# Optimization experiments

Measured on AMD Instinct MI355X. Metric: run time of the kernel, lower is better.

## Reference

```python
import jax, jax.numpy as jnp
import numpy as np

C, D, K, N, R = 96, 192, 4, 16, 6  # d_model, d_inner, directions, d_state, dt_rank
B, H, W = 8, 64, 64


def _ln(x, w, b):
    mu = x.mean(-1, keepdims=True)
    var = ((x - mu) ** 2).mean(-1, keepdims=True)
    return (x - mu) * jax.lax.rsqrt(var + 1e-5) * w + b


def setup_inputs() -> dict:
    key = jax.random.key(0)
    ks = jax.random.split(key, 16)
    s = 0.02
    A = jnp.tile(jnp.arange(1, N + 1, dtype=jnp.float32)[None, None, :], (K, D, 1))
    return {
        "x": jax.random.normal(ks[0], (B, C, H, W), jnp.float32),
        "ln1_w": jnp.ones((C,), jnp.float32),
        "ln1_b": jnp.zeros((C,), jnp.float32),
        "in_proj_w": jax.random.normal(ks[1], (2 * D, C), jnp.float32) * s,
        "conv_w": jax.random.normal(ks[2], (D, 1, 3, 3), jnp.float32) * s,
        "conv_b": jnp.zeros((D,), jnp.float32),
        "x_proj_w": jax.random.normal(ks[3], (K, R + 2 * N, D), jnp.float32) * s,
        "dt_projs_w": jax.random.normal(ks[4], (K, D, R), jnp.float32) * s,
        "dt_projs_b": jax.random.normal(ks[5], (K, D), jnp.float32) * 0.1,
        "A_logs": jnp.log(A),
        "Ds": jnp.ones((K, D), jnp.float32),
        "out_norm_w": jnp.ones((D,), jnp.float32),
        "out_norm_b": jnp.zeros((D,), jnp.float32),
        "out_proj_w": jax.random.normal(ks[6], (C, D), jnp.float32) * s,
        "pm_norm_w": jnp.ones((4 * C,), jnp.float32),
        "pm_norm_b": jnp.zeros((4 * C,), jnp.float32),
        "pm_red_w": jax.random.normal(ks[7], (2 * C, 4 * C), jnp.float32) * s,
    }


def reference(x, ln1_w, ln1_b, in_proj_w, conv_w, conv_b, x_proj_w, dt_projs_w,
              dt_projs_b, A_logs, Ds, out_norm_w, out_norm_b, out_proj_w,
              pm_norm_w, pm_norm_b, pm_red_w):
    b, c, h, w = x.shape
    L = h * w
    xh = jnp.transpose(x, (0, 2, 3, 1))  # [B,H,W,C]
    resid = xh
    xn = _ln(xh, ln1_w, ln1_b)
    xz = xn @ in_proj_w.T  # [B,H,W,2D]
    xp, z = xz[..., :D], xz[..., D:]
    xc = jnp.transpose(xp, (0, 3, 1, 2))  # [B,D,H,W]
    xc = jax.lax.conv_general_dilated(
        xc, conv_w, (1, 1), ((1, 1), (1, 1)),
        dimension_numbers=("NCHW", "OIHW", "NCHW"), feature_group_count=D)
    xc = jax.nn.silu(xc + conv_b[None, :, None, None])
    # cross-scan: row-major, col-major, and their reverses -> [B,K,D,L]
    xf = xc.reshape(b, D, L)
    xt = jnp.transpose(xc, (0, 1, 3, 2)).reshape(b, D, L)
    xs = jnp.stack([xf, xt, xf[..., ::-1], xt[..., ::-1]], axis=1)
    x_dbl = jnp.einsum("bkdl,kcd->bkcl", xs, x_proj_w)
    dts = jnp.einsum("bkrl,kdr->bkdl", x_dbl[:, :, :R], dt_projs_w)
    Bs = x_dbl[:, :, R:R + N]  # [B,K,N,L]
    Cs = x_dbl[:, :, R + N:R + 2 * N]
    delta = jax.nn.softplus(dts + dt_projs_b[None, :, :, None])  # [B,K,D,L]
    A = -jnp.exp(A_logs)  # [K,D,N]
    dT = jnp.transpose(delta, (3, 0, 1, 2))  # [L,B,K,D]
    uT = jnp.transpose(xs, (3, 0, 1, 2))
    BT = jnp.transpose(Bs, (3, 0, 1, 2))  # [L,B,K,N]
    CT = jnp.transpose(Cs, (3, 0, 1, 2))
    h0 = jnp.zeros((b, K, D, N), x.dtype)

    def step(hst, inp):
        dt, ut, bt, ct = inp
        hst = hst * jnp.exp(dt[..., None] * A) + (dt * ut)[..., None] * bt[:, :, None, :]
        return hst, jnp.einsum("bkdn,bkn->bkd", hst, ct)

    _, yT = jax.lax.scan(step, h0, (dT, uT, BT, CT))  # yT: [L,B,K,D]
    y = jnp.transpose(yT, (1, 2, 3, 0)) + Ds[None, :, :, None] * xs  # [B,K,D,L]

    def unT(v):  # undo col-major traversal
        return jnp.transpose(v.reshape(b, D, w, h), (0, 1, 3, 2)).reshape(b, D, L)

    yc = y[:, 0] + y[:, 2, :, ::-1] + unT(y[:, 1]) + unT(y[:, 3, :, ::-1])
    yo = jnp.transpose(yc.reshape(b, D, h, w), (0, 2, 3, 1))  # [B,H,W,D]
    yo = _ln(yo, out_norm_w, out_norm_b) * jax.nn.silu(z)
    out = resid + yo @ out_proj_w.T  # [B,H,W,C]
    # PatchMerging2D
    x0 = out[:, 0::2, 0::2]
    x1 = out[:, 1::2, 0::2]
    x2 = out[:, 0::2, 1::2]
    x3 = out[:, 1::2, 1::2]
    xm = jnp.concatenate([x0, x1, x2, x3], -1)  # [B,H/2,W/2,4C]
    xm = _ln(xm, pm_norm_w, pm_norm_b) @ pm_red_w.T  # [B,H/2,W/2,2C]
    return jnp.transpose(xm, (0, 3, 1, 2))
```

## Files before the change

kernel.cpp:

```cpp
#include <hip/hip_runtime.h>
#include <hip/hip_bf16.h>


__device__ __forceinline__ float sigm(float x){ return 1.f/(1.f+__expf(-x)); }
__device__ __forceinline__ float softplus_(float x){ return (x>20.f)? x : __logf(1.f+__expf(x)); }

__device__ __forceinline__ int perm_kl(int k, int v){
  if(k==0) return v;
  if(k==1) return ((v&63)<<6)|(v>>6);
  if(k==2) return 4095-v;
  int m = 4095-v; return ((m&63)<<6)|(m>>6);
}

__global__ __launch_bounds__(256) void k0_prep(
    const float* __restrict__ ipw, const float* __restrict__ xpw,
    const float* __restrict__ dtw, const float* __restrict__ opw,
    const float* __restrict__ pmw,
    float* __restrict__ ipwT, float* __restrict__ xpwTp,
    float* __restrict__ dtwT, float* __restrict__ opwT,
    float* __restrict__ pmwT)
{
  int g = blockIdx.x*256 + threadIdx.x;
  if(g < 36864){
    int c = g/384, n = g%384;
    ipwT[g] = ipw[n*96 + c];
  } else if(g < 67584){
    int t = g - 36864; int dd = t/160, n = t - dd*160; int k = n/40, c = n - k*40;
    float v;
    if(c < 6)       v = xpw[(k*38 + c)*192 + dd];
    else if(c < 8)  v = 0.f;
    else            v = xpw[(k*38 + (c-2))*192 + dd];
    xpwTp[t] = v;
  } else if(g < 72192){
    int t = g - 67584; int kr = t/192, d = t - kr*192; int k = kr/6, r = kr - k*6;
    dtwT[t] = dtw[(k*192 + d)*6 + r];
  } else if(g < 90624){
    int t = g - 72192; int d = t/96, c = t - d*96;
    opwT[t] = opw[c*192 + d];
  } else if(g < 164352){
    int t = g - 90624; int n = t/192, c2 = t - n*192;
    pmwT[t] = pmw[c2*384 + n];
  }
}

#define XT_PAD 68
__global__ __launch_bounds__(256) void k1_ln_inproj(
    const float* __restrict__ x, const float* __restrict__ lnw, const float* __restrict__ lnb,
    const float* __restrict__ ipwT, float* __restrict__ xT,
    float* __restrict__ xp, float* __restrict__ z)
{
  __shared__ float xt[96*XT_PAD];
  __shared__ float lnw_s[96], lnb_s[96], mu_s[64], rs_s[64];
  int tid = threadIdx.x;
  int mt = blockIdx.x, nt = blockIdx.y, b = blockIdx.z;
  int g0 = mt*64;
  const float* xb = x + (size_t)b*96*4096 + g0;
  for(int idx=tid; idx<6144; idx+=256){
    int c = idx>>6, p = idx&63;
    xt[c*XT_PAD+p] = xb[c*4096 + p];
  }
  if(tid<96){ lnw_s[tid]=lnw[tid]; lnb_s[tid]=lnb[tid]; }
  __syncthreads();
  if(nt==0){
    float* xTb = xT + ((size_t)(b*4096 + g0))*96;
    for(int idx=tid; idx<6144; idx+=256){
      int p = idx/96, c = idx - p*96;
      xTb[idx] = xt[c*XT_PAD+p];
    }
  }
  if(tid<64){
    float s=0.f,q=0.f;
    for(int c=0;c<96;c++){ float v=xt[c*XT_PAD+tid]; s+=v; q+=v*v; }
    float mu = s*(1.f/96.f);
    mu_s[tid]=mu; rs_s[tid]=rsqrtf(q*(1.f/96.f)-mu*mu+1e-5f);
  }
  __syncthreads();
  for(int idx=tid; idx<6144; idx+=256){
    int c = idx>>6, p = idx&63;
    int a = c*XT_PAD+p;
    xt[a] = (xt[a]-mu_s[p])*rs_s[p]*lnw_s[c]+lnb_s[c];
  }
  __syncthreads();
  int tm = tid>>5, tn = tid&31;
  float acc[8][4];
  #pragma unroll
  for(int i=0;i<8;i++){acc[i][0]=0.f;acc[i][1]=0.f;acc[i][2]=0.f;acc[i][3]=0.f;}
  const float* wbase = ipwT + nt*128 + tn*4;
  for(int kk=0;kk<96;kk++){
    float4 w4 = *(const float4*)(wbase + kk*384);
    float4 a0 = *(const float4*)&xt[kk*XT_PAD + tm*8];
    float4 a1 = *(const float4*)&xt[kk*XT_PAD + tm*8 + 4];
    float av[8]={a0.x,a0.y,a0.z,a0.w,a1.x,a1.y,a1.z,a1.w};
    #pragma unroll
    for(int i=0;i<8;i++){
      acc[i][0]=fmaf(av[i],w4.x,acc[i][0]);
      acc[i][1]=fmaf(av[i],w4.y,acc[i][1]);
      acc[i][2]=fmaf(av[i],w4.z,acc[i][2]);
      acc[i][3]=fmaf(av[i],w4.w,acc[i][3]);
    }
  }
  int n = nt*128 + tn*4;
  #pragma unroll
  for(int i=0;i<8;i++){
    size_t row = (size_t)(b*4096 + g0 + tm*8 + i);
    float4 v = make_float4(acc[i][0],acc[i][1],acc[i][2],acc[i][3]);
    if(n < 192) *(float4*)(xp + row*192 + n) = v;
    else        *(float4*)(z  + row*192 + (n-192)) = v;
  }
}

__global__ __launch_bounds__(192) void k2_conv(
    const float* __restrict__ xp, const float* __restrict__ cw, const float* __restrict__ cb,
    float* __restrict__ xc)
{
  __shared__ float cw_s[1728];
  int tid = threadIdx.x;
  int pq = blockIdx.x, b = blockIdx.y;
  for(int i=tid;i<1728;i+=192) cw_s[i]=cw[i];
  __syncthreads();
  int p0 = pq*4;
  int h = p0>>6, w0 = p0&63;
  const float* base = xp + (size_t)b*4096*192 + tid;
  const float* wp = &cw_s[tid*9];
  float bias = cb[tid];
  float acc[4] = {bias,bias,bias,bias};
  #pragma unroll
  for(int ky=0;ky<3;ky++){
    int hh = h+ky-1;
    if(hh<0||hh>63) continue;
    float v[6];
    #pragma unroll
    for(int xx=0;xx<6;xx++){
      int ww = w0-1+xx;
      v[xx] = (ww>=0 && ww<64) ? base[((size_t)(hh*64+ww))*192] : 0.f;
    }
    float wk0=wp[ky*3], wk1=wp[ky*3+1], wk2=wp[ky*3+2];
    #pragma unroll
    for(int j=0;j<4;j++)
      acc[j] = fmaf(v[j],wk0, fmaf(v[j+1],wk1, fmaf(v[j+2],wk2, acc[j])));
  }
  #pragma unroll
  for(int j=0;j<4;j++){
    float a = acc[j];
    a = a * sigm(a);
    xc[((size_t)(b*4096)+p0+j)*192 + tid] = a;
  }
}

__global__ __launch_bounds__(320) void k3_proj(
    const float* __restrict__ xc, const float* __restrict__ xpwTp,
    float* __restrict__ xdbl)
{
  __shared__ float sm[32*192];
  int tid = threadIdx.x;
  int mt = blockIdx.x, b = blockIdx.y;
  int g0 = mt*32;
  const float* xcb = xc + ((size_t)(b*4096 + g0))*192;
  for(int idx=tid; idx<6144; idx+=320) sm[idx] = xcb[idx];
  __syncthreads();
  int tn = tid%40, tm = tid/40;
  float acc[4][4];
  #pragma unroll
  for(int i=0;i<4;i++){acc[i][0]=0.f;acc[i][1]=0.f;acc[i][2]=0.f;acc[i][3]=0.f;}
  const float* wb = xpwTp + tn*4;
  for(int kk=0;kk<192;kk+=2){
    float4 w0 = *(const float4*)(wb + kk*160);
    float4 w1 = *(const float4*)(wb + (kk+1)*160);
    #pragma unroll
    for(int i=0;i<4;i++){
      float2 a = *(const float2*)&sm[(tm*4+i)*192 + kk];
      acc[i][0] = fmaf(a.x,w0.x, fmaf(a.y,w1.x, acc[i][0]));
      acc[i][1] = fmaf(a.x,w0.y, fmaf(a.y,w1.y, acc[i][1]));
      acc[i][2] = fmaf(a.x,w0.z, fmaf(a.y,w1.z, acc[i][2]));
      acc[i][3] = fmaf(a.x,w0.w, fmaf(a.y,w1.w, acc[i][3]));
    }
  }
  #pragma unroll
  for(int i=0;i<4;i++){
    *(float4*)(xdbl + ((size_t)(b*4096 + g0 + tm*4 + i))*160 + tn*4)
      = make_float4(acc[i][0],acc[i][1],acc[i][2],acc[i][3]);
  }
}

__global__ __launch_bounds__(192) void k4a_scanlocal(
    const float* __restrict__ xdbl, const float* __restrict__ xc,
    const float* __restrict__ alog, const float* __restrict__ dtwT,
    const float* __restrict__ dtb,
    float* __restrict__ localH, float* __restrict__ decayT)
{
  int d = threadIdx.x;
  int ch = blockIdx.x, k = blockIdx.y, b = blockIdx.z;
  __shared__ float dtw_s[6*192];
  #pragma unroll
  for(int r=0;r<6;r++) dtw_s[r*192+d] = dtwT[(k*6+r)*192+d];
  __syncthreads();
  float A[16];
  {
    const float4* ap = (const float4*)(alog + (k*192+d)*16);
    float4 a0=ap[0],a1=ap[1],a2=ap[2],a3=ap[3];
    float t[16]={a0.x,a0.y,a0.z,a0.w,a1.x,a1.y,a1.z,a1.w,a2.x,a2.y,a2.z,a2.w,a3.x,a3.y,a3.z,a3.w};
    #pragma unroll
    for(int n=0;n<16;n++) A[n] = -__expf(t[n]);
  }
  bool fast = true;
  #pragma unroll
  for(int n=1;n<16;n++)
    fast = fast && (fabsf(A[n] - (float)(n+1)*A[0]) <= 1e-4f*(float)(n+1)*fabsf(A[0]));
  float dtbv = dtb[k*192+d];
  float h[16];
  #pragma unroll
  for(int n=0;n<16;n++) h[n]=0.f;
  float S=0.f;
  const float* xb = xc + (size_t)b*4096*192 + d;
  size_t prow = (size_t)b*4096;
  for(int i=0;i<64;i++){
    int p = perm_kl(k, ch*64+i);
    const float* row = xdbl + (prow+p)*160 + k*40;
    float u = xb[(size_t)p*192];
    float delta = dtbv;
    #pragma unroll
    for(int r=0;r<6;r++) delta = fmaf(row[r], dtw_s[r*192+d], delta);
    delta = softplus_(delta);
    float4 B0=*(const float4*)(row+8),  B1=*(const float4*)(row+12),
           B2=*(const float4*)(row+16), B3=*(const float4*)(row+20);
    float Bn[16]={B0.x,B0.y,B0.z,B0.w,B1.x,B1.y,B1.z,B1.w,B2.x,B2.y,B2.z,B2.w,B3.x,B3.y,B3.z,B3.w};
    float du = delta*u;
    S += delta;
    if(fast){
      float e1 = __expf(delta*A[0]);
      float e = e1;
      #pragma unroll
      for(int n=0;n<16;n++){ h[n] = fmaf(h[n], e, du*Bn[n]); e *= e1; }
    } else {
      #pragma unroll
      for(int n=0;n<16;n++) h[n] = fmaf(h[n], __expf(delta*A[n]), du*Bn[n]);
    }
  }
  float dec[16];
  if(fast){
    float s1 = __expf(S*A[0]);
    float e = s1;
    #pragma unroll
    for(int n=0;n<16;n++){ dec[n]=e; e*=s1; }
  } else {
    #pragma unroll
    for(int n=0;n<16;n++) dec[n] = __expf(A[n]*S);
  }
  float* lh = localH + ((((size_t)(b*4+k))*64 + ch)*192 + d)*16;
  float* dt = decayT + ((((size_t)(b*4+k))*64 + ch)*192 + d)*16;
  #pragma unroll
  for(int n4=0;n4<4;n4++){
    *(float4*)(lh + n4*4) = make_float4(h[n4*4],h[n4*4+1],h[n4*4+2],h[n4*4+3]);
    *(float4*)(dt + n4*4) = make_float4(dec[n4*4],dec[n4*4+1],dec[n4*4+2],dec[n4*4+3]);
  }
}

__global__ __launch_bounds__(256) void k4b_chain(
    float* __restrict__ localH, const float* __restrict__ decayT)
{
  int g = blockIdx.x*256 + threadIdx.x;
  int bk = g/3072, dn = g - bk*3072;
  float hv = 0.f;
  size_t base = (size_t)bk*64*3072 + dn;
  for(int ch=0; ch<64; ch++){
    size_t idx = base + (size_t)ch*3072;
    float loc = localH[idx], dec = decayT[idx];
    localH[idx] = hv;
    hv = fmaf(hv, dec, loc);
  }
}

__global__ __launch_bounds__(192) void k4c_scanfull(
    const float* __restrict__ xdbl, const float* __restrict__ xc,
    const float* __restrict__ alog, const float* __restrict__ dtwT,
    const float* __restrict__ dtb, const float* __restrict__ hin,
    const float* __restrict__ Dsv, float* __restrict__ yB)
{
  int d = threadIdx.x;
  int ch = blockIdx.x, k = blockIdx.y, b = blockIdx.z;
  __shared__ float dtw_s[6*192];
  #pragma unroll
  for(int r=0;r<6;r++) dtw_s[r*192+d] = dtwT[(k*6+r)*192+d];
  __syncthreads();
  float A[16];
  {
    const float4* ap = (const float4*)(alog + (k*192+d)*16);
    float4 a0=ap[0],a1=ap[1],a2=ap[2],a3=ap[3];
    float t[16]={a0.x,a0.y,a0.z,a0.w,a1.x,a1.y,a1.z,a1.w,a2.x,a2.y,a2.z,a2.w,a3.x,a3.y,a3.z,a3.w};
    #pragma unroll
    for(int n=0;n<16;n++) A[n] = -__expf(t[n]);
  }
  bool fast = true;
  #pragma unroll
  for(int n=1;n<16;n++)
    fast = fast && (fabsf(A[n] - (float)(n+1)*A[0]) <= 1e-4f*(float)(n+1)*fabsf(A[0]));
  float dtbv = dtb[k*192+d];
  float h[16];
  {
    const float4* hp = (const float4*)(hin + ((((size_t)(b*4+k))*64 + ch)*192 + d)*16);
    float4 h0=hp[0],h1=hp[1],h2=hp[2],h3=hp[3];
    h[0]=h0.x;h[1]=h0.y;h[2]=h0.z;h[3]=h0.w;h[4]=h1.x;h[5]=h1.y;h[6]=h1.z;h[7]=h1.w;
    h[8]=h2.x;h[9]=h2.y;h[10]=h2.z;h[11]=h2.w;h[12]=h3.x;h[13]=h3.y;h[14]=h3.z;h[15]=h3.w;
  }
  float dsv = Dsv[k*192+d];
  const float* xb = xc + (size_t)b*4096*192 + d;
  size_t prow = (size_t)b*4096;
  size_t rbase = ((size_t)(b*4+k))*4096 + ch*64;
  float* yP = yB + rbase*192 + d;
  for(int i=0;i<64;i++){
    int p = perm_kl(k, ch*64+i);
    const float* row = xdbl + (prow+p)*160 + k*40;
    float u = xb[(size_t)p*192];
    float delta = dtbv;
    #pragma unroll
    for(int r=0;r<6;r++) delta = fmaf(row[r], dtw_s[r*192+d], delta);
    delta = softplus_(delta);
    float4 B0=*(const float4*)(row+8),  B1=*(const float4*)(row+12),
           B2=*(const float4*)(row+16), B3=*(const float4*)(row+20);
    float Bn[16]={B0.x,B0.y,B0.z,B0.w,B1.x,B1.y,B1.z,B1.w,B2.x,B2.y,B2.z,B2.w,B3.x,B3.y,B3.z,B3.w};
    float4 C0=*(const float4*)(row+24), C1=*(const float4*)(row+28),
           C2=*(const float4*)(row+32), C3=*(const float4*)(row+36);
    float Cn[16]={C0.x,C0.y,C0.z,C0.w,C1.x,C1.y,C1.z,C1.w,C2.x,C2.y,C2.z,C2.w,C3.x,C3.y,C3.z,C3.w};
    float du = delta*u;
    float y = 0.f;
    if(fast){
      float e1 = __expf(delta*A[0]);
      float e = e1;
      #pragma unroll
      for(int n=0;n<16;n++){ h[n] = fmaf(h[n], e, du*Bn[n]); y = fmaf(h[n], Cn[n], y); e *= e1; }
    } else {
      #pragma unroll
      for(int n=0;n<16;n++){ h[n] = fmaf(h[n], __expf(delta*A[n]), du*Bn[n]); y = fmaf(h[n], Cn[n], y); }
    }
    yP[(size_t)i*192] = fmaf(dsv, u, y);
  }
}

#define YPAD 193
__global__ __launch_bounds__(256) void k5_combine(
    const float* __restrict__ yS, const float* __restrict__ z, const float* __restrict__ xT,
    const float* __restrict__ onw, const float* __restrict__ onb,
    const float* __restrict__ opwT, float* __restrict__ out_pre)
{
  __shared__ float yn[64*YPAD];
  __shared__ float wsm[48*96];
  __shared__ float mu_s[64], rs_s[64];
  int tid = threadIdx.x;
  int mt = blockIdx.x, b = blockIdx.y;
  int g0 = mt*64;
  size_t base = (size_t)b*4*4096;
  for(int idx=tid; idx<12288; idx+=256){
    int p = idx/192, d = idx - p*192;
    int gp = g0 + p;
    int l1 = ((gp&63)<<6)|(gp>>6);
    float v = yS[(base + gp)*192 + d]
            + yS[(base + 4096 + l1)*192 + d]
            + yS[(base + 2*4096 + (4095-gp))*192 + d]
            + yS[(base + 3*4096 + (4095-l1))*192 + d];
    yn[p*YPAD+d] = v;
  }
  __syncthreads();
  {
    int p = tid>>2, q = tid&3;
    float s=0.f, sq=0.f;
    for(int c=q;c<192;c+=4){ float v=yn[p*YPAD+c]; s+=v; sq=fmaf(v,v,sq); }
    s  += __shfl_xor(s,1);  sq += __shfl_xor(sq,1);
    s  += __shfl_xor(s,2);  sq += __shfl_xor(sq,2);
    if(q==0){
      float mu = s*(1.f/192.f);
      mu_s[p]=mu; rs_s[p]=rsqrtf(sq*(1.f/192.f)-mu*mu+1e-5f);
    }
  }
  __syncthreads();
  for(int idx=tid; idx<12288; idx+=256){
    int p = idx/192, d = idx - p*192;
    float zz = z[((size_t)(b*4096+g0+p))*192 + d];
    float v = (yn[p*YPAD+d]-mu_s[p])*rs_s[p]*onw[d]+onb[d];
    yn[p*YPAD+d] = v * zz * sigm(zz);
  }
  __syncthreads();
  int tn = tid&15, tm = tid>>4;
  float acc[4][6];
  #pragma unroll
  for(int i=0;i<4;i++)
    #pragma unroll
    for(int j=0;j<6;j++) acc[i][j]=0.f;
  for(int kc=0; kc<4; kc++){
    for(int idx=tid; idx<4608; idx+=256) wsm[idx] = opwT[kc*4608 + idx];
    __syncthreads();
    for(int kk=0;kk<48;kk++){
      float a0 = yn[(tm*4+0)*YPAD + kc*48+kk];
      float a1 = yn[(tm*4+1)*YPAD + kc*48+kk];
      float a2 = yn[(tm*4+2)*YPAD + kc*48+kk];
      float a3 = yn[(tm*4+3)*YPAD + kc*48+kk];
      const float* wr = &wsm[kk*96 + tn*6];
      #pragma unroll
      for(int j=0;j<6;j++){
        float w = wr[j];
        acc[0][j]=fmaf(a0,w,acc[0][j]);
        acc[1][j]=fmaf(a1,w,acc[1][j]);
        acc[2][j]=fmaf(a2,w,acc[2][j]);
        acc[3][j]=fmaf(a3,w,acc[3][j]);
      }
    }
    __syncthreads();
  }
  #pragma unroll
  for(int i=0;i<4;i++){
    size_t row = (size_t)(b*4096 + g0 + tm*4 + i);
    const float* xr = xT + row*96 + tn*6;
    float* orr = out_pre + row*96 + tn*6;
    #pragma unroll
    for(int j=0;j<6;j++) orr[j] = acc[i][j] + xr[j];
  }
}

__global__ __launch_bounds__(192) void k6_pm(
    const float* __restrict__ out_pre, const float* __restrict__ pmw, const float* __restrict__ pmb,
    const float* __restrict__ pmwT, float* __restrict__ outp)
{
  __shared__ float xm[8*388];
  __shared__ float xo[8*193];
  __shared__ float mus[8], rss[8];
  int tid = threadIdx.x;
  int jt = blockIdx.x, i = blockIdx.y, b = blockIdx.z;
  for(int idx=tid; idx<3072; idx+=192){
    int pj = idx/384, n = idx - pj*384;
    int q = n/96, c = n - q*96;
    int j = jt*8 + pj;
    int h2 = 2*i + (q&1), w2 = 2*j + (q>>1);
    xm[pj*388+n] = out_pre[((size_t)b*4096 + h2*64 + w2)*96 + c];
  }
  __syncthreads();
  if(tid<8){
    float s=0.f,q=0.f;
    for(int n=0;n<384;n++){ float v=xm[tid*388+n]; s+=v; q+=v*v; }
    float mu=s*(1.f/384.f);
    mus[tid]=mu; rss[tid]=rsqrtf(q*(1.f/384.f)-mu*mu+1e-5f);
  }
  __syncthreads();
  for(int idx=tid; idx<3072; idx+=192){
    int pj = idx/384, n = idx - pj*384;
    xm[pj*388+n] = (xm[pj*388+n]-mus[pj])*rss[pj]*pmw[n]+pmb[n];
  }
  __syncthreads();
  float acc[8];
  #pragma unroll
  for(int pj=0;pj<8;pj++) acc[pj]=0.f;
  const float* wb = pmwT + tid;
  for(int n4=0;n4<96;n4++){
    float w0=wb[(n4*4+0)*192], w1=wb[(n4*4+1)*192], w2=wb[(n4*4+2)*192], w3=wb[(n4*4+3)*192];
    #pragma unroll
    for(int pj=0;pj<8;pj++){
      float4 v = *(const float4*)&xm[pj*388 + n4*4];
      acc[pj] = fmaf(v.x,w0,fmaf(v.y,w1,fmaf(v.z,w2,fmaf(v.w,w3,acc[pj]))));
    }
  }
  #pragma unroll
  for(int pj=0;pj<8;pj++) xo[pj*193+tid]=acc[pj];
  __syncthreads();
  for(int idx=tid; idx<1536; idx+=192){
    int c2 = idx>>3, pj = idx&7;
    outp[(((size_t)b*192 + c2)*32 + i)*32 + jt*8 + pj] = xo[pj*193+c2];
  }
}

extern "C" void kernel_launch(void* const* d_in, const int* in_sizes, int n_in,
                              void* d_out, int out_size, void* d_ws, size_t ws_size,
                              hipStream_t stream)
{
  const float* x    = (const float*)d_in[0];
  const float* lnw  = (const float*)d_in[1];
  const float* lnb  = (const float*)d_in[2];
  const float* ipw  = (const float*)d_in[3];
  const float* cw   = (const float*)d_in[4];
  const float* cb   = (const float*)d_in[5];
  const float* xpw  = (const float*)d_in[6];
  const float* dtw  = (const float*)d_in[7];
  const float* dtb  = (const float*)d_in[8];
  const float* alog = (const float*)d_in[9];
  const float* Dsv  = (const float*)d_in[10];
  const float* onw  = (const float*)d_in[11];
  const float* onb  = (const float*)d_in[12];
  const float* opw  = (const float*)d_in[13];
  const float* pmnw = (const float*)d_in[14];
  const float* pmnb = (const float*)d_in[15];
  const float* pmrw = (const float*)d_in[16];
  float* out = (float*)d_out;

  float* ws    = (float*)d_ws;
  float* xT    = ws;
  float* xpb   = xT + 3145728;
  float* zb    = xpb + 6291456;
  float* xcb   = zb + 6291456;
  float* yB    = xcb + 6291456;
  float* lH    = yB + 25165824;
  float* dT    = lH + 6291456;
  float* ipwT  = dT + 6291456;
  float* xpwTp = ipwT + 36864;
  float* dtwT  = xpwTp + 30720;
  float* opwT  = dtwT + 4608;
  float* pmwT  = opwT + 18432;
  float* xdbl  = xpb;
  float* outp  = xpb;

  k0_prep      <<<dim3(642),     dim3(256), 0, stream>>>(ipw,xpw,dtw,opw,pmrw, ipwT,xpwTp,dtwT,opwT,pmwT);
  k1_ln_inproj <<<dim3(64,3,8),  dim3(256), 0, stream>>>(x,lnw,lnb,ipwT, xT,xpb,zb);
  k2_conv      <<<dim3(1024,8),  dim3(192), 0, stream>>>(xpb,cw,cb, xcb);
  k3_proj      <<<dim3(128,8),   dim3(320), 0, stream>>>(xcb,xpwTp, xdbl);
  k4a_scanlocal<<<dim3(64,4,8),  dim3(192), 0, stream>>>(xdbl,xcb,alog,dtwT,dtb, lH,dT);
  k4b_chain    <<<dim3(384),     dim3(256), 0, stream>>>(lH,dT);
  k4c_scanfull <<<dim3(64,4,8),  dim3(192), 0, stream>>>(xdbl,xcb,alog,dtwT,dtb,lH,Dsv, yB);
  k5_combine   <<<dim3(64,8),    dim3(256), 0, stream>>>(yB,zb,xT,onw,onb,opwT, outp);
  k6_pm        <<<dim3(4,32,8),  dim3(192), 0, stream>>>(outp,pmnw,pmnb,pmwT, out);
}
```

Measured before the change: 359.8 us.

## Stage scan rows in shared memory, prefetch u, and shorten exp/dot dependency chains

Both chunked scan kernels now cooperatively load their 64 permuted x_dbl rows (dt, B, C) into shared memory up front, rather than each thread re-reading them from global memory. u values are prefetched four steps ahead, and the dt weights are held in registers. The serial power chain for the decay factors is replaced by a log-depth expansion, and the C dot product is split into four partial sums. This targets per-step global-load latency and long serial FMA dependency chains. In exchange it uses more registers and shared memory, which could reduce occupancy.

```diff
diff --git a/kernel.cpp b/kernel.cpp
--- a/kernel.cpp
+++ b/kernel.cpp
@@ -182,18 +182,30 @@
   }
 }
 
+#define EXPAND_E(e, f1)                                                     \
+    float f2=(f1)*(f1), f4=f2*f2, f8=f4*f4;                                 \
+    e[0]=(f1); e[1]=f2; e[2]=f2*(f1); e[3]=f4; e[4]=f4*(f1); e[5]=f4*f2;    \
+    e[6]=f4*e[2]; e[7]=f8; e[8]=f8*(f1); e[9]=f8*f2; e[10]=f8*e[2];         \
+    e[11]=f8*f4; e[12]=f8*e[4]; e[13]=f8*e[5]; e[14]=f8*e[6]; e[15]=f8*f8;
+
 __global__ __launch_bounds__(192) void k4a_scanlocal(
     const float* __restrict__ xdbl, const float* __restrict__ xc,
     const float* __restrict__ alog, const float* __restrict__ dtwT,
     const float* __restrict__ dtb,
     float* __restrict__ localH, float* __restrict__ decayT)
 {
+  __shared__ float rows[64*40];
   int d = threadIdx.x;
   int ch = blockIdx.x, k = blockIdx.y, b = blockIdx.z;
-  __shared__ float dtw_s[6*192];
-  #pragma unroll
-  for(int r=0;r<6;r++) dtw_s[r*192+d] = dtwT[(k*6+r)*192+d];
-  __syncthreads();
+  size_t prow = (size_t)b*4096;
+  for(int idx=d; idx<2560; idx+=192){
+    int i = idx/40, c = idx - i*40;
+    int p = perm_kl(k, ch*64+i);
+    rows[idx] = xdbl[(prow+p)*160 + k*40 + c];
+  }
+  float w0=dtwT[(k*6+0)*192+d], w1=dtwT[(k*6+1)*192+d], w2=dtwT[(k*6+2)*192+d],
+        w3=dtwT[(k*6+3)*192+d], w4=dtwT[(k*6+4)*192+d], w5=dtwT[(k*6+5)*192+d];
+  float dtbv = dtb[k*192+d];
   float A[16];
   {
     const float4* ap = (const float4*)(alog + (k*192+d)*16);
@@ -206,42 +218,52 @@
   #pragma unroll
   for(int n=1;n<16;n++)
     fast = fast && (fabsf(A[n] - (float)(n+1)*A[0]) <= 1e-4f*(float)(n+1)*fabsf(A[0]));
-  float dtbv = dtb[k*192+d];
   float h[16];
   #pragma unroll
   for(int n=0;n<16;n++) h[n]=0.f;
   float S=0.f;
   const float* xb = xc + (size_t)b*4096*192 + d;
-  size_t prow = (size_t)b*4096;
-  for(int i=0;i<64;i++){
-    int p = perm_kl(k, ch*64+i);
-    const float* row = xdbl + (prow+p)*160 + k*40;
-    float u = xb[(size_t)p*192];
-    float delta = dtbv;
-    #pragma unroll
-    for(int r=0;r<6;r++) delta = fmaf(row[r], dtw_s[r*192+d], delta);
-    delta = softplus_(delta);
-    float4 B0=*(const float4*)(row+8),  B1=*(const float4*)(row+12),
-           B2=*(const float4*)(row+16), B3=*(const float4*)(row+20);
-    float Bn[16]={B0.x,B0.y,B0.z,B0.w,B1.x,B1.y,B1.z,B1.w,B2.x,B2.y,B2.z,B2.w,B3.x,B3.y,B3.z,B3.w};
-    float du = delta*u;
-    S += delta;
-    if(fast){
-      float e1 = __expf(delta*A[0]);
-      float e = e1;
+  float u[4];
+  #pragma unroll
+  for(int j=0;j<4;j++) u[j] = xb[(size_t)perm_kl(k,ch*64+j)*192];
+  __syncthreads();
+  for(int ib=0; ib<64; ib+=4){
+    float nu[4]={0.f,0.f,0.f,0.f};
+    if(ib<60){
       #pragma unroll
-      for(int n=0;n<16;n++){ h[n] = fmaf(h[n], e, du*Bn[n]); e *= e1; }
-    } else {
+      for(int j=0;j<4;j++) nu[j] = xb[(size_t)perm_kl(k,ch*64+ib+4+j)*192];
+    }
+    #pragma unroll
+    for(int j=0;j<4;j++){
+      const float* row = &rows[(ib+j)*40];
+      float p01 = fmaf(row[1],w1, row[0]*w0);
+      float p23 = fmaf(row[3],w3, row[2]*w2);
+      float p45 = fmaf(row[5],w5, row[4]*w4);
+      float delta = softplus_((dtbv + p01) + (p23 + p45));
+      float du = delta*u[j];
+      S += delta;
+      float4 B0=*(const float4*)(row+8),  B1=*(const float4*)(row+12),
+             B2=*(const float4*)(row+16), B3=*(const float4*)(row+20);
+      float Bn[16]={B0.x,B0.y,B0.z,B0.w,B1.x,B1.y,B1.z,B1.w,
+                    B2.x,B2.y,B2.z,B2.w,B3.x,B3.y,B3.z,B3.w};
+      float e[16];
+      if(fast){
+        float f1=__expf(delta*A[0]);
+        EXPAND_E(e, f1)
+      } else {
+        #pragma unroll
+        for(int n=0;n<16;n++) e[n]=__expf(delta*A[n]);
+      }
       #pragma unroll
-      for(int n=0;n<16;n++) h[n] = fmaf(h[n], __expf(delta*A[n]), du*Bn[n]);
-    }
+      for(int n=0;n<16;n++) h[n] = fmaf(h[n], e[n], du*Bn[n]);
+    }
+    #pragma unroll
+    for(int j=0;j<4;j++) u[j]=nu[j];
   }
   float dec[16];
   if(fast){
     float s1 = __expf(S*A[0]);
-    float e = s1;
-    #pragma unroll
-    for(int n=0;n<16;n++){ dec[n]=e; e*=s1; }
+    EXPAND_E(dec, s1)
   } else {
     #pragma unroll
     for(int n=0;n<16;n++) dec[n] = __expf(A[n]*S);
@@ -276,12 +298,18 @@
     const float* __restrict__ dtb, const float* __restrict__ hin,
     const float* __restrict__ Dsv, float* __restrict__ yB)
 {
+  __shared__ float rows[64*40];
   int d = threadIdx.x;
   int ch = blockIdx.x, k = blockIdx.y, b = blockIdx.z;
-  __shared__ float dtw_s[6*192];
-  #pragma unroll
-  for(int r=0;r<6;r++) dtw_s[r*192+d] = dtwT[(k*6+r)*192+d];
-  __syncthreads();
+  size_t prow = (size_t)b*4096;
+  for(int idx=d; idx<2560; idx+=192){
+    int i = idx/40, c = idx - i*40;
+    int p = perm_kl(k, ch*64+i);
+    rows[idx] = xdbl[(prow+p)*160 + k*40 + c];
+  }
+  float w0=dtwT[(k*6+0)*192+d], w1=dtwT[(k*6+1)*192+d], w2=dtwT[(k*6+2)*192+d],
+        w3=dtwT[(k*6+3)*192+d], w4=dtwT[(k*6+4)*192+d], w5=dtwT[(k*6+5)*192+d];
+  float dtbv = dtb[k*192+d];
   float A[16];
   {
     const float4* ap = (const float4*)(alog + (k*192+d)*16);
@@ -294,7 +322,6 @@
   #pragma unroll
   for(int n=1;n<16;n++)
     fast = fast && (fabsf(A[n] - (float)(n+1)*A[0]) <= 1e-4f*(float)(n+1)*fabsf(A[0]));
-  float dtbv = dtb[k*192+d];
   float h[16];
   {
     const float4* hp = (const float4*)(hin + ((((size_t)(b*4+k))*64 + ch)*192 + d)*16);
@@ -304,35 +331,58 @@
   }
   float dsv = Dsv[k*192+d];
   const float* xb = xc + (size_t)b*4096*192 + d;
-  size_t prow = (size_t)b*4096;
   size_t rbase = ((size_t)(b*4+k))*4096 + ch*64;
   float* yP = yB + rbase*192 + d;
-  for(int i=0;i<64;i++){
-    int p = perm_kl(k, ch*64+i);
-    const float* row = xdbl + (prow+p)*160 + k*40;
-    float u = xb[(size_t)p*192];
-    float delta = dtbv;
-    #pragma unroll
-    for(int r=0;r<6;r++) delta = fmaf(row[r], dtw_s[r*192+d], delta);
-    delta = softplus_(delta);
-    float4 B0=*(const float4*)(row+8),  B1=*(const float4*)(row+12),
-           B2=*(const float4*)(row+16), B3=*(const float4*)(row+20);
-    float Bn[16]={B0.x,B0.y,B0.z,B0.w,B1.x,B1.y,B1.z,B1.w,B2.x,B2.y,B2.z,B2.w,B3.x,B3.y,B3.z,B3.w};
-    float4 C0=*(const float4*)(row+24), C1=*(const float4*)(row+28),
-           C2=*(const float4*)(row+32), C3=*(const float4*)(row+36);
-    float Cn[16]={C0.x,C0.y,C0.z,C0.w,C1.x,C1.y,C1.z,C1.w,C2.x,C2.y,C2.z,C2.w,C3.x,C3.y,C3.z,C3.w};
-    float du = delta*u;
-    float y = 0.f;
-    if(fast){
-      float e1 = __expf(delta*A[0]);
-      float e = e1;
+  float u[4];
+  #pragma unroll
+  for(int j=0;j<4;j++) u[j] = xb[(size_t)perm_kl(k,ch*64+j)*192];
+  __syncthreads();
+  float S=0.f;
+  for(int ib=0; ib<64; ib+=4){
+    float nu[4]={0.f,0.f,0.f,0.f};
+    if(ib<60){
       #pragma unroll
-      for(int n=0;n<16;n++){ h[n] = fmaf(h[n], e, du*Bn[n]); y = fmaf(h[n], Cn[n], y); e *= e1; }
-    } else {
+      for(int j=0;j<4;j++) nu[j] = xb[(size_t)perm_kl(k,ch*64+ib+4+j)*192];
+    }
+    #pragma unroll
+    for(int j=0;j<4;j++){
+      const float* row = &rows[(ib+j)*40];
+      float p01 = fmaf(row[1],w1, row[0]*w0);
+      float p23 = fmaf(row[3],w3, row[2]*w2);
+      float p45 = fmaf(row[5],w5, row[4]*w4);
+      float delta = softplus_((dtbv + p01) + (p23 + p45));
+      float du = delta*u[j];
+      S += delta;
+      float4 B0=*(const float4*)(row+8),  B1=*(const float4*)(row+12),
+             B2=*(const float4*)(row+16), B3=*(const float4*)(row+20);
+      float Bn[16]={B0.x,B0.y,B0.z,B0.w,B1.x,B1.y,B1.z,B1.w,
+                    B2.x,B2.y,B2.z,B2.w,B3.x,B3.y,B3.z,B3.w};
+      float4 C0=*(const float4*)(row+24), C1=*(const float4*)(row+28),
+             C2=*(const float4*)(row+32), C3=*(const float4*)(row+36);
+      float Cn[16]={C0.x,C0.y,C0.z,C0.w,C1.x,C1.y,C1.z,C1.w,
+                    C2.x,C2.y,C2.z,C2.w,C3.x,C3.y,C3.z,C3.w};
+      float e[16];
+      if(fast){
+        float f1=__expf(delta*A[0]);
+        EXPAND_E(e, f1)
+      } else {
+        #pragma unroll
+        for(int n=0;n<16;n++) e[n]=__expf(delta*A[n]);
+      }
       #pragma unroll
-      for(int n=0;n<16;n++){ h[n] = fmaf(h[n], __expf(delta*A[n]), du*Bn[n]); y = fmaf(h[n], Cn[n], y); }
-    }
-    yP[(size_t)i*192] = fmaf(dsv, u, y);
+      for(int n=0;n<16;n++) h[n] = fmaf(h[n], e[n], du*Bn[n]);
+      float y0=0.f,y1=0.f,y2=0.f,y3=0.f;
+      #pragma unroll
+      for(int n=0;n<4;n++){
+        y0 = fmaf(h[n],    Cn[n],    y0);
+        y1 = fmaf(h[n+4],  Cn[n+4],  y1);
+        y2 = fmaf(h[n+8],  Cn[n+8],  y2);
+        y3 = fmaf(h[n+12], Cn[n+12], y3);
+      }
+      yP[(size_t)(ib+j)*192] = fmaf(dsv, u[j], (y0+y1)+(y2+y3));
+    }
+    #pragma unroll
+    for(int j=0;j<4;j++) u[j]=nu[j];
   }
 }
 
```

New measurement: 430.4 us. +19.6%, slower.

## Stage per-chunk xdbl rows in shared memory and shorten scan dependency chains

Applied to the files above, without the earlier changes.

Both scan kernels now copy the chunk's 64 xdbl rows (40 floats each) into shared memory cooperatively before the loop, instead of every thread reading the same rows from global memory. The permutation is replaced by a start offset plus stride, so the u pointer advances by a fixed step. The dt weights move into registers. In the fast path the power chain for the decay is split into four parallel chains and the y reduction into four partial sums, which shortens the serial dependency latency. The cost is more shared memory per block and duplicated fast and slow loop bodies.

```diff
diff --git a/kernel.cpp b/kernel.cpp
--- a/kernel.cpp
+++ b/kernel.cpp
@@ -5,11 +5,13 @@
 __device__ __forceinline__ float sigm(float x){ return 1.f/(1.f+__expf(-x)); }
 __device__ __forceinline__ float softplus_(float x){ return (x>20.f)? x : __logf(1.f+__expf(x)); }
 
-__device__ __forceinline__ int perm_kl(int k, int v){
-  if(k==0) return v;
-  if(k==1) return ((v&63)<<6)|(v>>6);
-  if(k==2) return 4095-v;
-  int m = 4095-v; return ((m&63)<<6)|(m>>6);
+__device__ __forceinline__ void scan_p0dp(int k, int ch, int& p0, int& dp){
+  switch(k){
+    case 0:  p0 = ch*64;        dp = 1;   break;
+    case 1:  p0 = ch;           dp = 64;  break;
+    case 2:  p0 = 4095 - ch*64; dp = -1;  break;
+    default: p0 = 4095 - ch;    dp = -64; break;
+  }
 }
 
 __global__ __launch_bounds__(256) void k0_prep(
@@ -188,61 +190,100 @@
     const float* __restrict__ dtb,
     float* __restrict__ localH, float* __restrict__ decayT)
 {
+  __shared__ float rows[64*40];
   int d = threadIdx.x;
   int ch = blockIdx.x, k = blockIdx.y, b = blockIdx.z;
-  __shared__ float dtw_s[6*192];
-  #pragma unroll
-  for(int r=0;r<6;r++) dtw_s[r*192+d] = dtwT[(k*6+r)*192+d];
-  __syncthreads();
-  float A[16];
+  size_t prow = (size_t)b*4096;
+  int p0, dp;
+  scan_p0dp(k, ch, p0, dp);
+  for(int idx4=d; idx4<640; idx4+=192){
+    int i = idx4/10, c4 = idx4 - i*10;
+    *(float4*)&rows[idx4*4] =
+      *(const float4*)(xdbl + (prow + (size_t)(p0 + i*dp))*160 + k*40 + c4*4);
+  }
+  float w0=dtwT[(k*6+0)*192+d], w1=dtwT[(k*6+1)*192+d], w2=dtwT[(k*6+2)*192+d],
+        w3=dtwT[(k*6+3)*192+d], w4=dtwT[(k*6+4)*192+d], w5=dtwT[(k*6+5)*192+d];
+  float dtbv = dtb[k*192+d];
+  float A0; bool fast = true;
   {
-    const float4* ap = (const float4*)(alog + (k*192+d)*16);
+    const float4* ap = (const float4*)(alog + (size_t)(k*192+d)*16);
     float4 a0=ap[0],a1=ap[1],a2=ap[2],a3=ap[3];
     float t[16]={a0.x,a0.y,a0.z,a0.w,a1.x,a1.y,a1.z,a1.w,a2.x,a2.y,a2.z,a2.w,a3.x,a3.y,a3.z,a3.w};
-    #pragma unroll
-    for(int n=0;n<16;n++) A[n] = -__expf(t[n]);
-  }
-  bool fast = true;
-  #pragma unroll
-  for(int n=1;n<16;n++)
-    fast = fast && (fabsf(A[n] - (float)(n+1)*A[0]) <= 1e-4f*(float)(n+1)*fabsf(A[0]));
-  float dtbv = dtb[k*192+d];
+    A0 = -__expf(t[0]);
+    #pragma unroll
+    for(int n=1;n<16;n++)
+      fast = fast && (fabsf(-__expf(t[n]) - (float)(n+1)*A0) <= 1e-4f*(float)(n+1)*fabsf(A0));
+  }
   float h[16];
   #pragma unroll
   for(int n=0;n<16;n++) h[n]=0.f;
   float S=0.f;
-  const float* xb = xc + (size_t)b*4096*192 + d;
-  size_t prow = (size_t)b*4096;
-  for(int i=0;i<64;i++){
-    int p = perm_kl(k, ch*64+i);
-    const float* row = xdbl + (prow+p)*160 + k*40;
-    float u = xb[(size_t)p*192];
-    float delta = dtbv;
-    #pragma unroll
-    for(int r=0;r<6;r++) delta = fmaf(row[r], dtw_s[r*192+d], delta);
-    delta = softplus_(delta);
-    float4 B0=*(const float4*)(row+8),  B1=*(const float4*)(row+12),
-           B2=*(const float4*)(row+16), B3=*(const float4*)(row+20);
-    float Bn[16]={B0.x,B0.y,B0.z,B0.w,B1.x,B1.y,B1.z,B1.w,B2.x,B2.y,B2.z,B2.w,B3.x,B3.y,B3.z,B3.w};
-    float du = delta*u;
-    S += delta;
-    if(fast){
-      float e1 = __expf(delta*A[0]);
-      float e = e1;
+  const float* xu = xc + (prow + (size_t)p0)*192 + d;
+  ptrdiff_t ustride = (ptrdiff_t)dp*192;
+  float dec[16];
+  __syncthreads();
+  if(fast){
+    for(int i=0;i<64;i++){
+      const float* row = &rows[i*40];
+      float u = *xu; xu += ustride;
+      float p01 = fmaf(row[1],w1, row[0]*w0);
+      float p23 = fmaf(row[3],w3, row[2]*w2);
+      float p45 = fmaf(row[5],w5, row[4]*w4);
+      float delta = softplus_((dtbv + p01) + (p23 + p45));
+      float du = delta*u;
+      S += delta;
+      float4 B0=*(const float4*)(row+8),  B1=*(const float4*)(row+12),
+             B2=*(const float4*)(row+16), B3=*(const float4*)(row+20);
+      float e1=__expf(delta*A0);
+      float e2=e1*e1;
+      float c0=e1, c1=e2, c2=e2*e1, e4=e2*e2, c3=e4;
+      h[0]=fmaf(h[0],c0,du*B0.x); h[1]=fmaf(h[1],c1,du*B0.y);
+      h[2]=fmaf(h[2],c2,du*B0.z); h[3]=fmaf(h[3],c3,du*B0.w);
+      c0*=e4; c1*=e4; c2*=e4; c3*=e4;
+      h[4]=fmaf(h[4],c0,du*B1.x); h[5]=fmaf(h[5],c1,du*B1.y);
+      h[6]=fmaf(h[6],c2,du*B1.z); h[7]=fmaf(h[7],c3,du*B1.w);
+      c0*=e4; c1*=e4; c2*=e4; c3*=e4;
+      h[8]=fmaf(h[8],c0,du*B2.x); h[9]=fmaf(h[9],c1,du*B2.y);
+      h[10]=fmaf(h[10],c2,du*B2.z); h[11]=fmaf(h[11],c3,du*B2.w);
+      c0*=e4; c1*=e4; c2*=e4; c3*=e4;
+      h[12]=fmaf(h[12],c0,du*B3.x); h[13]=fmaf(h[13],c1,du*B3.y);
+      h[14]=fmaf(h[14],c2,du*B3.z); h[15]=fmaf(h[15],c3,du*B3.w);
+    }
+    float s1=__expf(S*A0);
+    float s2=s1*s1;
+    float c0=s1, c1=s2, c2=s2*s1, s4=s2*s2, c3=s4;
+    dec[0]=c0; dec[1]=c1; dec[2]=c2; dec[3]=c3;
+    c0*=s4; c1*=s4; c2*=s4; c3*=s4;
+    dec[4]=c0; dec[5]=c1; dec[6]=c2; dec[7]=c3;
+    c0*=s4; c1*=s4; c2*=s4; c3*=s4;
+    dec[8]=c0; dec[9]=c1; dec[10]=c2; dec[11]=c3;
+    c0*=s4; c1*=s4; c2*=s4; c3*=s4;
+    dec[12]=c0; dec[13]=c1; dec[14]=c2; dec[15]=c3;
+  } else {
+    float A[16];
+    {
+      const float4* ap = (const float4*)(alog + (size_t)(k*192+d)*16);
+      float4 a0=ap[0],a1=ap[1],a2=ap[2],a3=ap[3];
+      float t[16]={a0.x,a0.y,a0.z,a0.w,a1.x,a1.y,a1.z,a1.w,a2.x,a2.y,a2.z,a2.w,a3.x,a3.y,a3.z,a3.w};
       #pragma unroll
-      for(int n=0;n<16;n++){ h[n] = fmaf(h[n], e, du*Bn[n]); e *= e1; }
-    } else {
+      for(int n=0;n<16;n++) A[n] = -__expf(t[n]);
+    }
+    for(int i=0;i<64;i++){
+      const float* row = &rows[i*40];
+      float u = *xu; xu += ustride;
+      float p01 = fmaf(row[1],w1, row[0]*w0);
+      float p23 = fmaf(row[3],w3, row[2]*w2);
+      float p45 = fmaf(row[5],w5, row[4]*w4);
+      float delta = softplus_((dtbv + p01) + (p23 + p45));
+      float du = delta*u;
+      S += delta;
+      float4 B0=*(const float4*)(row+8),  B1=*(const float4*)(row+12),
+             B2=*(const float4*)(row+16), B3=*(const float4*)(row+20);
+      float Bn[16]={B0.x,B0.y,B0.z,B0.w,B1.x,B1.y,B1.z,B1.w,
+                    B2.x,B2.y,B2.z,B2.w,B3.x,B3.y,B3.z,B3.w};
       #pragma unroll
       for(int n=0;n<16;n++) h[n] = fmaf(h[n], __expf(delta*A[n]), du*Bn[n]);
     }
-  }
-  float dec[16];
-  if(fast){
-    float s1 = __expf(S*A[0]);
-    float e = s1;
-    #pragma unroll
-    for(int n=0;n<16;n++){ dec[n]=e; e*=s1; }
-  } else {
     #pragma unroll
     for(int n=0;n<16;n++) dec[n] = __expf(A[n]*S);
   }
@@ -276,25 +317,30 @@
     const float* __restrict__ dtb, const float* __restrict__ hin,
     const float* __restrict__ Dsv, float* __restrict__ yB)
 {
+  __shared__ float rows[64*40];
   int d = threadIdx.x;
   int ch = blockIdx.x, k = blockIdx.y, b = blockIdx.z;
-  __shared__ float dtw_s[6*192];
-  #pragma unroll
-  for(int r=0;r<6;r++) dtw_s[r*192+d] = dtwT[(k*6+r)*192+d];
-  __syncthreads();
-  float A[16];
+  size_t prow = (size_t)b*4096;
+  int p0, dp;
+  scan_p0dp(k, ch, p0, dp);
+  for(int idx4=d; idx4<640; idx4+=192){
+    int i = idx4/10, c4 = idx4 - i*10;
+    *(float4*)&rows[idx4*4] =
+      *(const float4*)(xdbl + (prow + (size_t)(p0 + i*dp))*160 + k*40 + c4*4);
+  }
+  float w0=dtwT[(k*6+0)*192+d], w1=dtwT[(k*6+1)*192+d], w2=dtwT[(k*6+2)*192+d],
+        w3=dtwT[(k*6+3)*192+d], w4=dtwT[(k*6+4)*192+d], w5=dtwT[(k*6+5)*192+d];
+  float dtbv = dtb[k*192+d];
+  float A0; bool fast = true;
   {
-    const float4* ap = (const float4*)(alog + (k*192+d)*16);
+    const float4* ap = (const float4*)(alog + (size_t)(k*192+d)*16);
     float4 a0=ap[0],a1=ap[1],a2=ap[2],a3=ap[3];
     float t[16]={a0.x,a0.y,a0.z,a0.w,a1.x,a1.y,a1.z,a1.w,a2.x,a2.y,a2.z,a2.w,a3.x,a3.y,a3.z,a3.w};
-    #pragma unroll
-    for(int n=0;n<16;n++) A[n] = -__expf(t[n]);
-  }
-  bool fast = true;
-  #pragma unroll
-  for(int n=1;n<16;n++)
-    fast = fast && (fabsf(A[n] - (float)(n+1)*A[0]) <= 1e-4f*(float)(n+1)*fabsf(A[0]));
-  float dtbv = dtb[k*192+d];
+    A0 = -__expf(t[0]);
+    #pragma unroll
+    for(int n=1;n<16;n++)
+      fast = fast && (fabsf(-__expf(t[n]) - (float)(n+1)*A0) <= 1e-4f*(float)(n+1)*fabsf(A0));
+  }
   float h[16];
   {
     const float4* hp = (const float4*)(hin + ((((size_t)(b*4+k))*64 + ch)*192 + d)*16);
@@ -303,36 +349,76 @@
     h[8]=h2.x;h[9]=h2.y;h[10]=h2.z;h[11]=h2.w;h[12]=h3.x;h[13]=h3.y;h[14]=h3.z;h[15]=h3.w;
   }
   float dsv = Dsv[k*192+d];
-  const float* xb = xc + (size_t)b*4096*192 + d;
-  size_t prow = (size_t)b*4096;
-  size_t rbase = ((size_t)(b*4+k))*4096 + ch*64;
-  float* yP = yB + rbase*192 + d;
-  for(int i=0;i<64;i++){
-    int p = perm_kl(k, ch*64+i);
-    const float* row = xdbl + (prow+p)*160 + k*40;
-    float u = xb[(size_t)p*192];
-    float delta = dtbv;
-    #pragma unroll
-    for(int r=0;r<6;r++) delta = fmaf(row[r], dtw_s[r*192+d], delta);
-    delta = softplus_(delta);
-    float4 B0=*(const float4*)(row+8),  B1=*(const float4*)(row+12),
-           B2=*(const float4*)(row+16), B3=*(const float4*)(row+20);
-    float Bn[16]={B0.x,B0.y,B0.z,B0.w,B1.x,B1.y,B1.z,B1.w,B2.x,B2.y,B2.z,B2.w,B3.x,B3.y,B3.z,B3.w};
-    float4 C0=*(const float4*)(row+24), C1=*(const float4*)(row+28),
-           C2=*(const float4*)(row+32), C3=*(const float4*)(row+36);
-    float Cn[16]={C0.x,C0.y,C0.z,C0.w,C1.x,C1.y,C1.z,C1.w,C2.x,C2.y,C2.z,C2.w,C3.x,C3.y,C3.z,C3.w};
-    float du = delta*u;
-    float y = 0.f;
-    if(fast){
-      float e1 = __expf(delta*A[0]);
-      float e = e1;
+  const float* xu = xc + (prow + (size_t)p0)*192 + d;
+  ptrdiff_t ustride = (ptrdiff_t)dp*192;
+  float* yP = yB + (((size_t)(b*4+k))*4096 + ch*64)*192 + d;
+  __syncthreads();
+  if(fast){
+    for(int i=0;i<64;i++){
+      const float* row = &rows[i*40];
+      float u = *xu; xu += ustride;
+      float p01 = fmaf(row[1],w1, row[0]*w0);
+      float p23 = fmaf(row[3],w3, row[2]*w2);
+      float p45 = fmaf(row[5],w5, row[4]*w4);
+      float delta = softplus_((dtbv + p01) + (p23 + p45));
+      float du = delta*u;
+      float4 B0=*(const float4*)(row+8),  B1=*(const float4*)(row+12),
+             B2=*(const float4*)(row+16), B3=*(const float4*)(row+20);
+      float4 C0=*(const float4*)(row+24), C1=*(const float4*)(row+28),
+             C2=*(const float4*)(row+32), C3=*(const float4*)(row+36);
+      float e1=__expf(delta*A0);
+      float e2=e1*e1;
+      float c0=e1, c1=e2, c2=e2*e1, e4=e2*e2, c3=e4;
+      h[0]=fmaf(h[0],c0,du*B0.x); h[1]=fmaf(h[1],c1,du*B0.y);
+      h[2]=fmaf(h[2],c2,du*B0.z); h[3]=fmaf(h[3],c3,du*B0.w);
+      float y0 = fmaf(h[0],C0.x, fmaf(h[1],C0.y, fmaf(h[2],C0.z, h[3]*C0.w)));
+      c0*=e4; c1*=e4; c2*=e4; c3*=e4;
+      h[4]=fmaf(h[4],c0,du*B1.x); h[5]=fmaf(h[5],c1,du*B1.y);
+      h[6]=fmaf(h[6],c2,du*B1.z); h[7]=fmaf(h[7],c3,du*B1.w);
+      float y1 = fmaf(h[4],C1.x, fmaf(h[5],C1.y, fmaf(h[6],C1.z, h[7]*C1.w)));
+      c0*=e4; c1*=e4; c2*=e4; c3*=e4;
+      h[8]=fmaf(h[8],c0,du*B2.x); h[9]=fmaf(h[9],c1,du*B2.y);
+      h[10]=fmaf(h[10],c2,du*B2.z); h[11]=fmaf(h[11],c3,du*B2.w);
+      float y2 = fmaf(h[8],C2.x, fmaf(h[9],C2.y, fmaf(h[10],C2.z, h[11]*C2.w)));
+      c0*=e4; c1*=e4; c2*=e4; c3*=e4;
+      h[12]=fmaf(h[12],c0,du*B3.x); h[13]=fmaf(h[13],c1,du*B3.y);
+      h[14]=fmaf(h[14],c2,du*B3.z); h[15]=fmaf(h[15],c3,du*B3.w);
+      float y3 = fmaf(h[12],C3.x, fmaf(h[13],C3.y, fmaf(h[14],C3.z, h[15]*C3.w)));
+      yP[(size_t)i*192] = fmaf(dsv, u, (y0+y1)+(y2+y3));
+    }
+  } else {
+    float A[16];
+    {
+      const float4* ap = (const float4*)(alog + (size_t)(k*192+d)*16);
+      float4 a0=ap[0],a1=ap[1],a2=ap[2],a3=ap[3];
+      float t[16]={a0.x,a0.y,a0.z,a0.w,a1.x,a1.y,a1.z,a1.w,a2.x,a2.y,a2.z,a2.w,a3.x,a3.y,a3.z,a3.w};
       #pragma unroll
-      for(int n=0;n<16;n++){ h[n] = fmaf(h[n], e, du*Bn[n]); y = fmaf(h[n], Cn[n], y); e *= e1; }
-    } else {
+      for(int n=0;n<16;n++) A[n] = -__expf(t[n]);
+    }
+    for(int i=0;i<64;i++){
+      const float* row = &rows[i*40];
+      float u = *xu; xu += ustride;
+      float p01 = fmaf(row[1],w1, row[0]*w0);
+      float p23 = fmaf(row[3],w3, row[2]*w2);
+      float p45 = fmaf(row[5],w5, row[4]*w4);
+      float delta = softplus_((dtbv + p01) + (p23 + p45));
+      float du = delta*u;
+      float4 B0=*(const float4*)(row+8),  B1=*(const float4*)(row+12),
+             B2=*(const float4*)(row+16), B3=*(const float4*)(row+20);
+      float Bn[16]={B0.x,B0.y,B0.z,B0.w,B1.x,B1.y,B1.z,B1.w,
+                    B2.x,B2.y,B2.z,B2.w,B3.x,B3.y,B3.z,B3.w};
+      float4 C0=*(const float4*)(row+24), C1=*(const float4*)(row+28),
+             C2=*(const float4*)(row+32), C3=*(const float4*)(row+36);
+      float Cn[16]={C0.x,C0.y,C0.z,C0.w,C1.x,C1.y,C1.z,C1.w,
+                    C2.x,C2.y,C2.z,C2.w,C3.x,C3.y,C3.z,C3.w};
+      float y = 0.f;
       #pragma unroll
-      for(int n=0;n<16;n++){ h[n] = fmaf(h[n], __expf(delta*A[n]), du*Bn[n]); y = fmaf(h[n], Cn[n], y); }
-    }
-    yP[(size_t)i*192] = fmaf(dsv, u, y);
+      for(int n=0;n<16;n++){
+        h[n] = fmaf(h[n], __expf(delta*A[n]), du*Bn[n]);
+        y = fmaf(h[n], Cn[n], y);
+      }
+      yP[(size_t)i*192] = fmaf(dsv, u, y);
+    }
   }
 }
 
```

Result: faster. 351.8 us (-2.2%).
